# Performance work log

Hardware: AMD Instinct MI355X
Metric: run time of the kernel (lower is better)

## Reference

```python
import jax, jax.numpy as jnp
import numpy as np

HE = 256  # encoder hidden
HD = 256  # decoder hidden


def _orthogonalize(enc):
    # Faithful to orthogonalize_encoder_inputs_new_new_new:
    # for each timestep i: buffer = x[i] - sum_{j<i} (x[i]*x[j])/(x[i]*x[i]) * x[i]
    # (all ops elementwise). The inner sum over j<i is an exclusive cumsum.
    x = jnp.transpose(enc, (1, 0, 2))                       # [T, B, H]
    s = jnp.cumsum(x, axis=0) - x                           # exclusive cumsum over j<i
    out = x - ((x * s) / (x * x)) * x                       # i=0: s=0 -> out=x
    return jnp.transpose(out, (0, 1, 2)), out               # keep [T,B,H] layout


def setup_inputs() -> dict:
    key = jax.random.key(0)
    k1, k2, k3, k4, k5 = jax.random.split(key, 5)
    B, TE, TD = 16, 128, 128
    # keras 'uniform' initializer = RandomUniform(-0.05, 0.05)
    return {
        "encoder_out_seq": jax.random.normal(k1, (B, TE, HE), dtype=jnp.float32),
        "decoder_out_seq": jax.random.normal(k2, (B, TD, HD), dtype=jnp.float32),
        "W_a": jax.random.uniform(k3, (HE, HE), jnp.float32, -0.05, 0.05),
        "U_a": jax.random.uniform(k4, (HD, HE), jnp.float32, -0.05, 0.05),
        "V_a": jax.random.uniform(k5, (HE, 1), jnp.float32, -0.05, 0.05),
    }


def reference(encoder_out_seq, decoder_out_seq, W_a, U_a, V_a):
    # Gram-Schmidt-style pass (math as in source; exactly vectorizable)
    x = jnp.transpose(encoder_out_seq, (1, 0, 2))           # [TE, B, H]
    s = jnp.cumsum(x, axis=0) - x                           # sum_{j<i} x[j]
    ortho = x - ((x * s) / (x * x)) * x                     # [TE, B, H]
    enc = jnp.transpose(ortho, (1, 0, 2))                   # [B, TE, H]

    # Bahdanau attention: the K.rnn steps carry no real state, so vectorize
    # over decoder time.
    was = jnp.einsum('beh,hk->bek', enc, W_a)               # [B, TE, H]
    uah = jnp.einsum('bdh,hk->bdk', decoder_out_seq, U_a)   # [B, TD, H]
    # tanh(S.Wa + h.Ua) . Va  -> energies [B, TD, TE]
    energy = jnp.einsum('bdeh,ho->bde',
                        jnp.tanh(was[:, None, :, :] + uah[:, :, None, :]),
                        V_a)
    e_outputs = jax.nn.softmax(energy, axis=-1)             # [B, TD, TE]
    c_outputs = jnp.einsum('bde,beh->bdh', e_outputs, enc)  # [B, TD, H]
    return c_outputs, e_outputs
```

## Files before the change

### kernel.cpp

```cpp
#include <hip/hip_runtime.h>
#include <cstddef>

#define Bq 16
#define TEq 128
#define TDq 128
#define Hq 256

#define kC2  2.8853900817779268f
#define kL2E 1.4426950408889634f

static __device__ __forceinline__ float fast_rcp(float x) {
#if __has_builtin(__builtin_amdgcn_rcpf)
    return __builtin_amdgcn_rcpf(x);
#else
    return 1.0f / x;
#endif
}

static __device__ __forceinline__ float fast_exp2(float x) {
#if __has_builtin(__builtin_amdgcn_exp2f)
    return __builtin_amdgcn_exp2f(x);
#else
    return exp2f(x);
#endif
}

__global__ __launch_bounds__(256) void k_ortho(const float* __restrict__ enc,
                                               float* __restrict__ out) {
    const int b = blockIdx.y;
    const int hg = blockIdx.x;
    const int tid = threadIdx.x;
    const int hl = tid & 31;
    const int ck = tid >> 5;
    const int h = (hg << 5) + hl;

    __shared__ float sums[8][33];

    const float* p = enc + ((size_t)b * TEq + ck * 16) * Hq + h;
    float xs[16];
#pragma unroll
    for (int i = 0; i < 16; ++i) xs[i] = p[(size_t)i * Hq];
    float tot = 0.0f;
#pragma unroll
    for (int i = 0; i < 16; ++i) tot += xs[i];
    sums[ck][hl] = tot;
    __syncthreads();

    float s = 0.0f;
    for (int c = 0; c < ck; ++c) s += sums[c][hl];

    float* q = out + ((size_t)b * TEq + ck * 16) * Hq + h;
#pragma unroll
    for (int i = 0; i < 16; ++i) {
        const float x = xs[i];
        const float r = (x * s) / (x * x);
        q[(size_t)i * Hq] = x - r * x;
        s += x;
    }
}

__global__ __launch_bounds__(256) void k_gemm2(const float* __restrict__ A0,
                                               const float* __restrict__ A1,
                                               const float* __restrict__ W0,
                                               const float* __restrict__ W1,
                                               float* __restrict__ Cw,
                                               float* __restrict__ Cu) {
    const int z = blockIdx.z;
    const float* __restrict__ A = z ? A1 : A0;
    const float* __restrict__ W = z ? W1 : W0;
    float* __restrict__ C = z ? Cu : Cw;
    const float scale = z ? 1.0f : kC2;

    const int bm = blockIdx.y * 32;
    const int bn = blockIdx.x * 64;

    __shared__ float sA[16][33];
    __shared__ float sB[16][64];

    const int tid = threadIdx.x;
    const int tx = tid & 15;
    const int ty = tid >> 4;
    const int arow = tid >> 3;
    const int akcol = (tid & 7) << 1;
    const int brow = tid >> 4;
    const int bcol = (tid & 15) << 2;

    float acc[2][4] = {};

    for (int k0 = 0; k0 < Hq; k0 += 16) {
        const float2 av = *(const float2*)(A + (size_t)(bm + arow) * Hq + k0 + akcol);
        const float4 bv = *(const float4*)(W + (size_t)(k0 + brow) * Hq + bn + bcol);
        __syncthreads();
        sA[akcol + 0][arow] = av.x;
        sA[akcol + 1][arow] = av.y;
        *(float4*)&sB[brow][bcol] = bv;
        __syncthreads();
#pragma unroll
        for (int k = 0; k < 16; ++k) {
            const float a0 = sA[k][ty << 1];
            const float a1 = sA[k][(ty << 1) + 1];
            const float4 b4 = *(const float4*)&sB[k][tx << 2];
            acc[0][0] = fmaf(a0, b4.x, acc[0][0]);
            acc[0][1] = fmaf(a0, b4.y, acc[0][1]);
            acc[0][2] = fmaf(a0, b4.z, acc[0][2]);
            acc[0][3] = fmaf(a0, b4.w, acc[0][3]);
            acc[1][0] = fmaf(a1, b4.x, acc[1][0]);
            acc[1][1] = fmaf(a1, b4.y, acc[1][1]);
            acc[1][2] = fmaf(a1, b4.z, acc[1][2]);
            acc[1][3] = fmaf(a1, b4.w, acc[1][3]);
        }
    }
#pragma unroll
    for (int i = 0; i < 2; ++i) {
        float4 o;
        o.x = acc[i][0] * scale;
        o.y = acc[i][1] * scale;
        o.z = acc[i][2] * scale;
        o.w = acc[i][3] * scale;
        *(float4*)(C + (size_t)(bm + (ty << 1) + i) * Hq + bn + (tx << 2)) = o;
    }
}

__global__ __launch_bounds__(256) void k_attn(const float* __restrict__ was,
                                              const float* __restrict__ uah,
                                              const float* __restrict__ enc_o,
                                              const float* __restrict__ Va,
                                              float* __restrict__ c_out,
                                              float* __restrict__ e_out) {
    const int b = blockIdx.y;
    const int d0 = blockIdx.x << 1;

    __shared__ float uahs[2][Hq];
    __shared__ float Vs[Hq];
    __shared__ float wts[2][TEq];

    const int tid = threadIdx.x;
    const int w = tid >> 6;
    const int lane = tid & 63;
    const int dl = w >> 1;
    const int half = w & 1;

    Vs[tid] = Va[tid];
#pragma unroll
    for (int j = 0; j < 2; ++j)
        uahs[j][tid] = uah[((size_t)b * TDq + d0 + j) * Hq + tid] * kC2;
    __syncthreads();

    const int g = lane >> 4;
    const int ll = lane & 15;

    float vs = Vs[lane] + Vs[lane + 64] + Vs[lane + 128] + Vs[lane + 192];
#pragma unroll
    for (int m = 1; m <= 32; m <<= 1) vs += __shfl_xor(vs, m);

    float4 ur[4], vr[4];
#pragma unroll
    for (int c = 0; c < 4; ++c) {
        ur[c] = *(const float4*)&uahs[dl][c * 64 + (ll << 2)];
        vr[c] = *(const float4*)&Vs[c * 64 + (ll << 2)];
    }

    const float* wasb = was + (size_t)b * TEq * Hq;

    for (int ei = 0; ei < 16; ++ei) {
        const int e = (half << 6) + (g << 4) + ei;
        const float* wp = wasb + (size_t)e * Hq + (ll << 2);
        float acc = 0.0f;
#pragma unroll
        for (int c = 0; c < 4; ++c) {
            const float4 wv = *(const float4*)(wp + c * 64);
            const float wf[4] = {wv.x, wv.y, wv.z, wv.w};
            const float uf[4] = {ur[c].x, ur[c].y, ur[c].z, ur[c].w};
            const float vf[4] = {vr[c].x, vr[c].y, vr[c].z, vr[c].w};
#pragma unroll
            for (int i = 0; i < 4; ++i) {
                const float s = wf[i] + uf[i];
                const float t = fast_exp2(s);
                const float r = fast_rcp(t + 1.0f);
                acc = fmaf(vf[i], r, acc);
            }
        }
        acc += __shfl_xor(acc, 1);
        acc += __shfl_xor(acc, 2);
        acc += __shfl_xor(acc, 4);
        acc += __shfl_xor(acc, 8);
        if (ll == 0) wts[dl][e] = vs - 2.0f * acc;
    }
    __syncthreads();

    if (w < 2) {
        const float v0 = wts[w][lane];
        const float v1 = wts[w][lane + 64];
        float mx = fmaxf(v0, v1);
#pragma unroll
        for (int m = 1; m <= 32; m <<= 1) mx = fmaxf(mx, __shfl_xor(mx, m));
        const float e0 = fast_exp2((v0 - mx) * kL2E);
        const float e1 = fast_exp2((v1 - mx) * kL2E);
        float sm = e0 + e1;
#pragma unroll
        for (int m = 1; m <= 32; m <<= 1) sm += __shfl_xor(sm, m);
        const float inv = fast_rcp(sm);
        const float w0 = e0 * inv;
        const float w1 = e1 * inv;
        wts[w][lane] = w0;
        wts[w][lane + 64] = w1;
        const size_t eb = ((size_t)b * TDq + d0 + w) * TEq;
        e_out[eb + lane] = w0;
        e_out[eb + lane + 64] = w1;
    }
    __syncthreads();

    float a0 = 0.0f, a1 = 0.0f;
    const float* ep = enc_o + (size_t)b * TEq * Hq + tid;
#pragma unroll 8
    for (int e = 0; e < TEq; ++e) {
        const float evv = ep[(size_t)e * Hq];
        a0 = fmaf(wts[0][e], evv, a0);
        a1 = fmaf(wts[1][e], evv, a1);
    }
    const size_t cb = ((size_t)b * TDq + d0) * Hq + tid;
    c_out[cb] = a0;
    c_out[cb + Hq] = a1;
}

extern "C" void kernel_launch(void* const* d_in, const int* in_sizes, int n_in,
                              void* d_out, int out_size, void* d_ws, size_t ws_size,
                              hipStream_t stream) {
    const float* enc = (const float*)d_in[0];
    const float* dec = (const float*)d_in[1];
    const float* Wa  = (const float*)d_in[2];
    const float* Ua  = (const float*)d_in[3];
    const float* Va  = (const float*)d_in[4];

    float* c_out = (float*)d_out;
    float* e_out = c_out + (size_t)Bq * TDq * Hq;

    float* enc_o = (float*)d_ws;
    float* wasb  = enc_o + (size_t)Bq * TEq * Hq;
    float* uahb  = wasb + (size_t)Bq * TEq * Hq;

    k_ortho<<<dim3(Hq / 32, Bq), dim3(256), 0, stream>>>(enc, enc_o);
    k_gemm2<<<dim3(Hq / 64, (Bq * TEq) / 32, 2), dim3(256), 0, stream>>>(
        enc_o, dec, Wa, Ua, wasb, uahb);
    k_attn<<<dim3(TDq / 2, Bq), dim3(256), 0, stream>>>(
        wasb, uahb, enc_o, Va, c_out, e_out);
}
```

Baseline: 106.2 us.

## Enlarge GEMM tile to 64x64 with register-prefetched B and vectorize context loop

The projection GEMM now uses 64x64 output tiles with a 4x4 per-thread microtile and a 32-wide K step. The B operand comes straight from global memory into registers and is double-buffered, so its shared-memory staging goes away. Separately, the context accumulation in the attention kernel reads its weights as float4 from shared memory. Together these aim to raise FMA density and cut LDS traffic in the GEMM, at the cost of more registers and half as many GEMM blocks.

Result: slower. 108.4 us (+2.0%).

```diff
diff --git a/kernel.cpp b/kernel.cpp
--- a/kernel.cpp
+++ b/kernel.cpp
@@ -71,53 +71,72 @@
     float* __restrict__ C = z ? Cu : Cw;
     const float scale = z ? 1.0f : kC2;
 
-    const int bm = blockIdx.y * 32;
+    const int bm = blockIdx.y * 64;
     const int bn = blockIdx.x * 64;
 
-    __shared__ float sA[16][33];
-    __shared__ float sB[16][64];
+    __shared__ float sA[32][68];
 
     const int tid = threadIdx.x;
     const int tx = tid & 15;
     const int ty = tid >> 4;
-    const int arow = tid >> 3;
-    const int akcol = (tid & 7) << 1;
-    const int brow = tid >> 4;
-    const int bcol = (tid & 15) << 2;
-
-    float acc[2][4] = {};
-
-    for (int k0 = 0; k0 < Hq; k0 += 16) {
-        const float2 av = *(const float2*)(A + (size_t)(bm + arow) * Hq + k0 + akcol);
-        const float4 bv = *(const float4*)(W + (size_t)(k0 + brow) * Hq + bn + bcol);
+    const int sr = tid & 63;
+    const int sc = (tid >> 6) << 2;
+
+    const float* __restrict__ Bp = W + bn + (tx << 2);
+    const float* __restrict__ Ap = A + (size_t)(bm + sr) * Hq;
+
+    float acc[4][4] = {};
+    float4 bcur[8], bnxt[8];
+
+#pragma unroll
+    for (int i = 0; i < 8; ++i)
+        bcur[i] = *(const float4*)(Bp + (size_t)i * Hq);
+
+    for (int kt = 0; kt < 8; ++kt) {
+        const int k0 = kt * 32;
+        const float4 a0 = *(const float4*)(Ap + k0 + sc);
+        const float4 a1 = *(const float4*)(Ap + k0 + sc + 16);
         __syncthreads();
-        sA[akcol + 0][arow] = av.x;
-        sA[akcol + 1][arow] = av.y;
-        *(float4*)&sB[brow][bcol] = bv;
+        sA[sc + 0][sr] = a0.x;  sA[sc + 1][sr] = a0.y;
+        sA[sc + 2][sr] = a0.z;  sA[sc + 3][sr] = a0.w;
+        sA[sc + 16][sr] = a1.x; sA[sc + 17][sr] = a1.y;
+        sA[sc + 18][sr] = a1.z; sA[sc + 19][sr] = a1.w;
         __syncthreads();
-#pragma unroll
-        for (int k = 0; k < 16; ++k) {
-            const float a0 = sA[k][ty << 1];
-            const float a1 = sA[k][(ty << 1) + 1];
-            const float4 b4 = *(const float4*)&sB[k][tx << 2];
-            acc[0][0] = fmaf(a0, b4.x, acc[0][0]);
-            acc[0][1] = fmaf(a0, b4.y, acc[0][1]);
-            acc[0][2] = fmaf(a0, b4.z, acc[0][2]);
-            acc[0][3] = fmaf(a0, b4.w, acc[0][3]);
-            acc[1][0] = fmaf(a1, b4.x, acc[1][0]);
-            acc[1][1] = fmaf(a1, b4.y, acc[1][1]);
-            acc[1][2] = fmaf(a1, b4.z, acc[1][2]);
-            acc[1][3] = fmaf(a1, b4.w, acc[1][3]);
+
+#pragma unroll
+        for (int kg = 0; kg < 4; ++kg) {
+            const int nk = k0 + kg * 8 + 8;
+            if (nk < Hq) {
+#pragma unroll
+                for (int i = 0; i < 8; ++i)
+                    bnxt[i] = *(const float4*)(Bp + (size_t)(nk + i) * Hq);
+            }
+#pragma unroll
+            for (int i = 0; i < 8; ++i) {
+                const float4 a4 = *(const float4*)&sA[kg * 8 + i][ty << 2];
+                const float af[4] = {a4.x, a4.y, a4.z, a4.w};
+                const float bf[4] = {bcur[i].x, bcur[i].y, bcur[i].z, bcur[i].w};
+#pragma unroll
+                for (int r = 0; r < 4; ++r)
+#pragma unroll
+                    for (int c = 0; c < 4; ++c)
+                        acc[r][c] = fmaf(af[r], bf[c], acc[r][c]);
+            }
+            if (nk < Hq) {
+#pragma unroll
+                for (int i = 0; i < 8; ++i) bcur[i] = bnxt[i];
+            }
         }
     }
-#pragma unroll
-    for (int i = 0; i < 2; ++i) {
+
+#pragma unroll
+    for (int r = 0; r < 4; ++r) {
         float4 o;
-        o.x = acc[i][0] * scale;
-        o.y = acc[i][1] * scale;
-        o.z = acc[i][2] * scale;
-        o.w = acc[i][3] * scale;
-        *(float4*)(C + (size_t)(bm + (ty << 1) + i) * Hq + bn + (tx << 2)) = o;
+        o.x = acc[r][0] * scale;
+        o.y = acc[r][1] * scale;
+        o.z = acc[r][2] * scale;
+        o.w = acc[r][3] * scale;
+        *(float4*)(C + (size_t)(bm + (ty << 2) + r) * Hq + bn + (tx << 2)) = o;
     }
 }
 
@@ -212,11 +231,18 @@
 
     float a0 = 0.0f, a1 = 0.0f;
     const float* ep = enc_o + (size_t)b * TEq * Hq + tid;
-#pragma unroll 8
-    for (int e = 0; e < TEq; ++e) {
-        const float evv = ep[(size_t)e * Hq];
-        a0 = fmaf(wts[0][e], evv, a0);
-        a1 = fmaf(wts[1][e], evv, a1);
+#pragma unroll 4
+    for (int e4 = 0; e4 < TEq; e4 += 4) {
+        const float4 w0v = *(const float4*)&wts[0][e4];
+        const float4 w1v = *(const float4*)&wts[1][e4];
+        const float x0 = ep[(size_t)(e4 + 0) * Hq];
+        const float x1 = ep[(size_t)(e4 + 1) * Hq];
+        const float x2 = ep[(size_t)(e4 + 2) * Hq];
+        const float x3 = ep[(size_t)(e4 + 3) * Hq];
+        a0 = fmaf(w0v.x, x0, a0); a1 = fmaf(w1v.x, x0, a1);
+        a0 = fmaf(w0v.y, x1, a0); a1 = fmaf(w1v.y, x1, a1);
+        a0 = fmaf(w0v.z, x2, a0); a1 = fmaf(w1v.z, x2, a1);
+        a0 = fmaf(w0v.w, x3, a0); a1 = fmaf(w1v.w, x3, a1);
     }
     const size_t cb = ((size_t)b * TDq + d0) * Hq + tid;
     c_out[cb] = a0;
@@ -240,7 +266,7 @@
     float* uahb  = wasb + (size_t)Bq * TEq * Hq;
 
     k_ortho<<<dim3(Hq / 32, Bq), dim3(256), 0, stream>>>(enc, enc_o);
-    k_gemm2<<<dim3(Hq / 64, (Bq * TEq) / 32, 2), dim3(256), 0, stream>>>(
+    k_gemm2<<<dim3(Hq / 64, (Bq * TEq) / 64, 2), dim3(256), 0, stream>>>(
         enc_o, dec, Wa, Ua, wasb, uahb);
     k_attn<<<dim3(TDq / 2, Bq), dim3(256), 0, stream>>>(
         wasb, uahb, enc_o, Va, c_out, e_out);
```
